# Kernel tuning notes

Measured on AMD Instinct MI355X. Metric: run time of the kernel, lower is better.

The kernel has to match this reference:

```python
import jax, jax.numpy as jnp
import numpy as np

Q_DIM = 1024
K_DIM = 1024
V_DIM = 1024
ATTEN_DIM = 1024
NUM_HEADS = 16
HEAD_DIM = ATTEN_DIM // NUM_HEADS
B, L = 4, 2048


def setup_inputs() -> dict:
    key = jax.random.key(0)
    ks = jax.random.split(key, 11)
    s = 0.02
    return {
        "query": jax.random.normal(ks[0], (B, L, Q_DIM), dtype=jnp.float32),
        "key":   jax.random.normal(ks[1], (B, L, K_DIM), dtype=jnp.float32),
        "value": jax.random.normal(ks[2], (B, L, V_DIM), dtype=jnp.float32),
        "Wq": jax.random.normal(ks[3], (Q_DIM, ATTEN_DIM), dtype=jnp.float32) * s,
        "bq": jnp.zeros((ATTEN_DIM,), dtype=jnp.float32),
        "Wk": jax.random.normal(ks[4], (K_DIM, ATTEN_DIM), dtype=jnp.float32) * s,
        "bk": jnp.zeros((ATTEN_DIM,), dtype=jnp.float32),
        "Wv": jax.random.normal(ks[5], (V_DIM, ATTEN_DIM), dtype=jnp.float32) * s,
        "bv": jnp.zeros((ATTEN_DIM,), dtype=jnp.float32),
        "Wo": jax.random.normal(ks[6], (ATTEN_DIM, V_DIM), dtype=jnp.float32) * s,
        "bo": jnp.zeros((V_DIM,), dtype=jnp.float32),
    }


def reference(query, key, value, Wq, bq, Wk, bk, Wv, bv, Wo, bo):
    # QKV projections
    q = query @ Wq + bq        # [B, L, A]
    k = key   @ Wk + bk        # [B, L, A]
    v = value @ Wv + bv        # [B, L, A]
    # split heads: [B, L, H, D]
    def split_heads(x):
        return x.reshape(x.shape[:-1] + (NUM_HEADS, HEAD_DIM))
    q, k, v = split_heads(q), split_heads(k), split_heads(v)
    scale = 1.0 / (HEAD_DIM ** 0.5)
    # scores: [B, H, Lq, Lk]
    scores = jnp.einsum("bqhd,bkhd->bhqk", q, k) * scale
    attn = jax.nn.softmax(scores, axis=-1)
    out = jnp.einsum("bhqk,bkhd->bqhd", attn, v)  # [B, Lq, H, D]
    out = out.reshape(out.shape[0], out.shape[1], ATTEN_DIM)
    return out @ Wo + bo
```

## Files before the change

kernel.cpp:

```cpp
#include <hip/hip_runtime.h>
#include <stdint.h>

#define L_SEQ 2048
#define BATCH 4
#define ADIM  1024
#define NH    16
#define HD    64

typedef __attribute__((ext_vector_type(8))) short bf16x8;
typedef __attribute__((ext_vector_type(4))) float f32x4;
typedef __attribute__((ext_vector_type(16))) float f32x16;
typedef __attribute__((ext_vector_type(2))) int i32x2;

__device__ __forceinline__ short f2bf(float f) {
    union { float f; unsigned u; } x; x.f = f;
    unsigned r = x.u + 0x7fffu + ((x.u >> 16) & 1u);
    return (short)(r >> 16);
}

__device__ __forceinline__ void async_ld16(void* lds, const void* g) {
    __builtin_amdgcn_global_load_lds(
        (const __attribute__((address_space(1))) void*)g,
        (__attribute__((address_space(3))) void*)lds, 16, 0, 0);
}

__device__ __forceinline__ int cvtpk_bf16(float a, float b) {
    int r;
    asm("v_cvt_pk_bf16_f32 %0, %1, %2" : "=v"(r) : "v"(a), "v"(b));
    return r;
}

__device__ __forceinline__ bf16x8 pack4(int a, int b, int c, int d) {
    union { int i[4]; bf16x8 v; } u;
    u.i[0] = a; u.i[1] = b; u.i[2] = c; u.i[3] = d;
    return u.v;
}

__global__ void cvt3_kernel(const float* __restrict__ s0, const float* __restrict__ s1,
                            const float* __restrict__ s2, short* __restrict__ dst, int n4) {
    int i = blockIdx.x * blockDim.x + threadIdx.x;
    if (i >= n4) return;
    int z = blockIdx.y;
    const float* src = (z == 0) ? s0 : (z == 1) ? s1 : s2;
    float4 v = reinterpret_cast<const float4*>(src)[i];
    short4 s;
    s.x = f2bf(v.x); s.y = f2bf(v.y); s.z = f2bf(v.z); s.w = f2bf(v.w);
    reinterpret_cast<short4*>(dst + (size_t)z * (BATCH * L_SEQ * ADIM))[i] = s;
}

__global__ void transpose4_kernel(const float* __restrict__ W0, const float* __restrict__ W1,
                                  const float* __restrict__ W2, const float* __restrict__ W3,
                                  short* __restrict__ outb) {
    __shared__ float t[32][33];
    int z = blockIdx.z;
    const float* in = (z == 0) ? W0 : (z == 1) ? W1 : (z == 2) ? W2 : W3;
    short* out = outb + (size_t)z * (ADIM * ADIM);
    int x  = blockIdx.x * 32 + threadIdx.x;
    int y0 = blockIdx.y * 32 + threadIdx.y;
#pragma unroll
    for (int j = 0; j < 4; ++j)
        t[threadIdx.y + 8 * j][threadIdx.x] = in[(y0 + 8 * j) * 1024 + x];
    __syncthreads();
    int x2 = blockIdx.y * 32 + threadIdx.x;
    int y2 = blockIdx.x * 32 + threadIdx.y;
#pragma unroll
    for (int j = 0; j < 4; ++j)
        out[(y2 + 8 * j) * 1024 + x2] = f2bf(t[threadIdx.x][threadIdx.y + 8 * j]);
}

__device__ __forceinline__ void gemm_core(const short* __restrict__ A,
                                          const short* __restrict__ BT,
                                          const float* __restrict__ bias,
                                          void* __restrict__ Cout,
                                          int mode, float scalemul,
                                          int m0, int n0) {
    const int K = 1024, N = 1024;
    __shared__ __align__(16) short smem[16384];
    int tid = threadIdx.x;
    int wave = tid >> 6, lane = tid & 63, quad = lane >> 4, l16 = lane & 15;
    int wm = wave & 1, wn = wave >> 1;
    f32x4 acc[4][4] = {};

    int row = tid >> 2, ck = tid & 3;
    const short* gA0 = A  + (size_t)(m0 + row) * K + ck * 8;
    const short* gA1 = gA0 + (size_t)64 * K;
    const short* gB0 = BT + (size_t)(n0 + row) * K + ck * 8;
    const short* gB1 = gB0 + (size_t)64 * K;
    int loA0 = tid * 8, loA1 = tid * 8 + 2048;
    int loB0 = tid * 8 + 4096, loB1 = tid * 8 + 6144;

    async_ld16(smem + loA0, gA0); async_ld16(smem + loA1, gA1);
    async_ld16(smem + loB0, gB0); async_ld16(smem + loB1, gB1);
    gA0 += 32; gA1 += 32; gB0 += 32; gB1 += 32;
    __syncthreads();

    int cur = 0;
    for (int t = 0; t < 32; ++t) {
        if (t < 31) {
            int off = (cur ^ 1) * 8192;
            async_ld16(smem + off + loA0, gA0); async_ld16(smem + off + loA1, gA1);
            async_ld16(smem + off + loB0, gB0); async_ld16(smem + off + loB1, gB1);
            gA0 += 32; gA1 += 32; gB0 += 32; gB1 += 32;
        }
        const short* Ab = smem + cur * 8192;
        const short* Bb = Ab + 4096;
        bf16x8 af[4], bfr[4];
#pragma unroll
        for (int mt = 0; mt < 4; ++mt)
            af[mt] = *(const bf16x8*)&Ab[(wm * 64 + mt * 16 + l16) * 32 + quad * 8];
#pragma unroll
        for (int nt = 0; nt < 4; ++nt)
            bfr[nt] = *(const bf16x8*)&Bb[(wn * 64 + nt * 16 + l16) * 32 + quad * 8];
#pragma unroll
        for (int mt = 0; mt < 4; ++mt)
#pragma unroll
            for (int nt = 0; nt < 4; ++nt)
                acc[mt][nt] = __builtin_amdgcn_mfma_f32_16x16x32_bf16(
                    af[mt], bfr[nt], acc[mt][nt], 0, 0, 0);
        __syncthreads();
        cur ^= 1;
    }

    if (mode == 0) {
#pragma unroll
        for (int nt = 0; nt < 4; ++nt) {
            int col = n0 + wn * 64 + nt * 16 + l16;
            float bv = bias[col];
#pragma unroll
            for (int mt = 0; mt < 4; ++mt)
#pragma unroll
                for (int r = 0; r < 4; ++r) {
                    int rw = m0 + wm * 64 + mt * 16 + quad * 4 + r;
                    ((short*)Cout)[(size_t)rw * N + col] = f2bf((acc[mt][nt][r] + bv) * scalemul);
                }
        }
    } else if (mode == 1) {
#pragma unroll
        for (int nt = 0; nt < 4; ++nt) {
            int col = n0 + wn * 64 + nt * 16 + l16;
            float bv = bias[col];
            int h = col >> 6, d = col & 63;
#pragma unroll
            for (int mt = 0; mt < 4; ++mt)
#pragma unroll
                for (int r = 0; r < 4; ++r) {
                    int rw = m0 + wm * 64 + mt * 16 + quad * 4 + r;
                    int b = rw >> 11, lk = rw & 2047;
                    ((short*)Cout)[(((size_t)b * NH + h) * HD + d) * L_SEQ + lk] =
                        f2bf(acc[mt][nt][r] + bv);
                }
        }
    } else {
#pragma unroll
        for (int nt = 0; nt < 4; ++nt) {
            int col = n0 + wn * 64 + nt * 16 + l16;
            float bv = bias[col];
#pragma unroll
            for (int mt = 0; mt < 4; ++mt)
#pragma unroll
                for (int r = 0; r < 4; ++r) {
                    int rw = m0 + wm * 64 + mt * 16 + quad * 4 + r;
                    ((float*)Cout)[(size_t)rw * N + col] = acc[mt][nt][r] + bv;
                }
        }
    }
}

__device__ __forceinline__ void gemm_swz(int& m0, int& n0) {
    int bid = blockIdx.y * 8 + blockIdx.x;
    int swz = (bid & 7) * 64 + (bid >> 3);
    n0 = (swz & 7) * 128;
    m0 = (swz >> 3) * 128;
}

__global__ __launch_bounds__(256, 4)
void gemm_one(const short* __restrict__ A, const short* __restrict__ BT,
              const float* __restrict__ bias, void* __restrict__ Cout,
              int mode, float scalemul) {
    int m0, n0; gemm_swz(m0, n0);
    gemm_core(A, BT, bias, Cout, mode, scalemul, m0, n0);
}

__global__ __launch_bounds__(256, 4)
void qkv_gemm(const short* __restrict__ Xbase, const short* __restrict__ WTbase,
              const float* __restrict__ bq, const float* __restrict__ bk,
              const float* __restrict__ bv,
              short* __restrict__ Qb, short* __restrict__ Kb, short* __restrict__ VTout,
              float qscale) {
    int z = blockIdx.z;
    const short* A  = Xbase + (size_t)z * (BATCH * L_SEQ * ADIM);
    const short* BT = WTbase + (size_t)z * (ADIM * ADIM);
    const float* bias = (z == 0) ? bq : (z == 1) ? bk : bv;
    void* out = (z == 0) ? (void*)Qb : (z == 1) ? (void*)Kb : (void*)VTout;
    int mode = (z == 2) ? 1 : 0;
    float sm = (z == 0) ? qscale : 1.0f;
    int m0, n0; gemm_swz(m0, n0);
    gemm_core(A, BT, bias, out, mode, sm, m0, n0);
}

__global__ __launch_bounds__(256, 4)
void attn_kernel(const short* __restrict__ Qb, const short* __restrict__ Kb,
                 const short* __restrict__ VT, short* __restrict__ Oout) {
    __shared__ __align__(16) short lds[16384];
    int tid = threadIdx.x;
    int wave = tid >> 6, lane = tid & 63;
    int r31 = lane & 31, hi = lane >> 5;

    int f = (blockIdx.z * NH + blockIdx.y) * (L_SEQ / 128) + blockIdx.x;
    int swz = (f & 7) * 128 + (f >> 3);
    int qb = swz & 15;
    int h  = (swz >> 4) & 15;
    int b  = swz >> 8;

    size_t qrow = (size_t)(b * L_SEQ + qb * 128 + wave * 32 + r31) * ADIM + h * HD;
    bf16x8 qf[4];
#pragma unroll
    for (int dc = 0; dc < 4; ++dc)
        qf[dc] = *(const bf16x8*)&Qb[qrow + dc * 16 + hi * 8];

    const short* Kbase = Kb + (size_t)b * L_SEQ * ADIM + h * HD;
    const short* Vbase = VT + ((size_t)(b * NH + h) * HD) * L_SEQ;
    const short* gp[4]; int step[4]; int ldso[4];
#pragma unroll
    for (int s = 0; s < 4; ++s) {
        int j = s * 256 + tid;
        ldso[s] = j * 8;
        if (j < 512) {
            int c = j >> 6, k = j & 63;
            gp[s] = Kbase + (size_t)k * ADIM + c * 8;
            step[s] = 64 * ADIM;
        } else {
            int jv = j - 512;
            int c = jv >> 6, d = jv & 63;
            gp[s] = Vbase + (size_t)d * L_SEQ + c * 8;
            step[s] = 64;
        }
    }

    f32x16 o0 = {}, o1 = {};
    f32x4 lp = {};

#pragma unroll
    for (int s = 0; s < 4; ++s) { async_ld16(lds + ldso[s], gp[s]); gp[s] += step[s]; }
    __syncthreads();

    int cur = 0;
    for (int t = 0; t < 32; ++t) {
        const short* kb_l = lds + cur * 8192;
        const short* vb_l = kb_l + 4096;
        if (t < 31) {
            short* dst = lds + (cur ^ 1) * 8192;
#pragma unroll
            for (int s = 0; s < 4; ++s) { async_ld16(dst + ldso[s], gp[s]); gp[s] += step[s]; }
        }
#pragma unroll
        for (int kt = 0; kt < 2; ++kt) {
            f32x16 sv = {};
            __builtin_amdgcn_s_setprio(1);
#pragma unroll
            for (int dc = 0; dc < 4; ++dc) {
                bf16x8 kf = *(const bf16x8*)&kb_l[(((dc << 1) + hi) * 64 + kt * 32 + r31) * 8];
                sv = __builtin_amdgcn_mfma_f32_32x32x16_bf16(kf, qf[dc], sv, 0, 0, 0);
            }
            __builtin_amdgcn_s_setprio(0);
#pragma unroll
            for (int r = 0; r < 16; ++r) sv[r] = __builtin_amdgcn_exp2f(sv[r]);
#pragma unroll
            for (int m = 0; m < 4; ++m)
#pragma unroll
                for (int j2 = 0; j2 < 4; ++j2) lp[j2] += sv[m * 4 + j2];

            int p0 = cvtpk_bf16(sv[0],  sv[1]);
            int p1 = cvtpk_bf16(sv[2],  sv[3]);
            int p2 = cvtpk_bf16(sv[4],  sv[5]);
            int p3 = cvtpk_bf16(sv[6],  sv[7]);
            int p4 = cvtpk_bf16(sv[8],  sv[9]);
            int p5 = cvtpk_bf16(sv[10], sv[11]);
            int p6 = cvtpk_bf16(sv[12], sv[13]);
            int p7 = cvtpk_bf16(sv[14], sv[15]);
            asm volatile("v_permlane32_swap_b32 %0, %1" : "+v"(p0), "+v"(p2));
            asm volatile("v_permlane32_swap_b32 %0, %1" : "+v"(p1), "+v"(p3));
            asm volatile("v_permlane32_swap_b32 %0, %1" : "+v"(p4), "+v"(p6));
            asm volatile("v_permlane32_swap_b32 %0, %1" : "+v"(p5), "+v"(p7));
            bf16x8 pf0 = pack4(p0, p1, p2, p3);
            bf16x8 pf1 = pack4(p4, p5, p6, p7);

            bf16x8 vf00 = *(const bf16x8*)&vb_l[((kt * 4 + hi)     * 64 + r31) * 8];
            bf16x8 vf01 = *(const bf16x8*)&vb_l[((kt * 4 + 2 + hi) * 64 + r31) * 8];
            bf16x8 vf10 = *(const bf16x8*)&vb_l[((kt * 4 + hi)     * 64 + 32 + r31) * 8];
            bf16x8 vf11 = *(const bf16x8*)&vb_l[((kt * 4 + 2 + hi) * 64 + 32 + r31) * 8];
            __builtin_amdgcn_s_setprio(1);
            o0 = __builtin_amdgcn_mfma_f32_32x32x16_bf16(vf00, pf0, o0, 0, 0, 0);
            o1 = __builtin_amdgcn_mfma_f32_32x32x16_bf16(vf10, pf0, o1, 0, 0, 0);
            o0 = __builtin_amdgcn_mfma_f32_32x32x16_bf16(vf01, pf1, o0, 0, 0, 0);
            o1 = __builtin_amdgcn_mfma_f32_32x32x16_bf16(vf11, pf1, o1, 0, 0, 0);
            __builtin_amdgcn_s_setprio(0);
        }
        __syncthreads();
        cur ^= 1;
    }

    float lsum = lp[0] + lp[1] + lp[2] + lp[3];
    lsum += __shfl_xor(lsum, 32);
    float inv = __builtin_amdgcn_rcpf(lsum);

    short* tile = lds + wave * (32 * 68);
#pragma unroll
    for (int dt = 0; dt < 2; ++dt)
#pragma unroll
        for (int g = 0; g < 4; ++g) {
            int d0 = dt * 32 + g * 8 + hi * 4;
            int pa, pb;
            if (dt == 0) {
                pa = cvtpk_bf16(o0[g * 4 + 0] * inv, o0[g * 4 + 1] * inv);
                pb = cvtpk_bf16(o0[g * 4 + 2] * inv, o0[g * 4 + 3] * inv);
            } else {
                pa = cvtpk_bf16(o1[g * 4 + 0] * inv, o1[g * 4 + 1] * inv);
                pb = cvtpk_bf16(o1[g * 4 + 2] * inv, o1[g * 4 + 3] * inv);
            }
            *(i32x2*)&tile[r31 * 68 + d0] = (i32x2){pa, pb};
        }
    __syncthreads();
    size_t obase = (size_t)(b * L_SEQ + qb * 128 + wave * 32) * ADIM + h * HD;
    int rr = lane >> 3, cc = lane & 7;
#pragma unroll
    for (int p = 0; p < 4; ++p) {
        int row = p * 8 + rr;
        bf16x8 v = *(const bf16x8*)&tile[row * 68 + cc * 8];
        *(bf16x8*)&Oout[obase + (size_t)row * ADIM + cc * 8] = v;
    }
}

extern "C" void kernel_launch(void* const* d_in, const int* in_sizes, int n_in,
                              void* d_out, int out_size, void* d_ws, size_t ws_size,
                              hipStream_t stream) {
    const float* query = (const float*)d_in[0];
    const float* keyp  = (const float*)d_in[1];
    const float* value = (const float*)d_in[2];
    const float* Wq = (const float*)d_in[3];
    const float* bq = (const float*)d_in[4];
    const float* Wk = (const float*)d_in[5];
    const float* bk = (const float*)d_in[6];
    const float* Wv = (const float*)d_in[7];
    const float* bv = (const float*)d_in[8];
    const float* Wo = (const float*)d_in[9];
    const float* bo = (const float*)d_in[10];

    const float QSCALE = 0.125f * 1.44269504f;
    const size_t MB = 1ull << 20;
    const int n4 = (BATCH * L_SEQ * ADIM) / 4;
    char* w = (char*)d_ws;
    dim3 tblk(32, 8);
    dim3 gemm_grid(ADIM / 128, (BATCH * L_SEQ) / 128);
    dim3 attn_grid(L_SEQ / 128, NH, BATCH);

    if (ws_size >= 104 * MB) {
        short* X0  = (short*)(w);
        short* WT  = (short*)(w + 48 * MB);
        short* VT  = (short*)(w + 56 * MB);
        short* Kb  = (short*)(w + 72 * MB);
        short* Qb  = (short*)(w + 88 * MB);
        short* AO  = X0;

        cvt3_kernel<<<dim3(n4 / 256, 3), 256, 0, stream>>>(query, keyp, value, X0, n4);
        transpose4_kernel<<<dim3(32, 32, 4), tblk, 0, stream>>>(Wq, Wk, Wv, Wo, WT);
        qkv_gemm<<<dim3(ADIM / 128, (BATCH * L_SEQ) / 128, 3), 256, 0, stream>>>(
            X0, WT, bq, bk, bv, Qb, Kb, VT, QSCALE);
        attn_kernel<<<attn_grid, 256, 0, stream>>>(Qb, Kb, VT, AO);
        gemm_one<<<gemm_grid, 256, 0, stream>>>(AO, WT + (size_t)3 * ADIM * ADIM, bo,
                                                d_out, 2, 1.0f);
    } else {
        short* X0  = (short*)(w);
        short* WT  = (short*)(w + 16 * MB);
        short* VT  = (short*)(w + 24 * MB);
        short* Kb  = (short*)(w + 40 * MB);
        short* Qb  = (short*)(w + 56 * MB);

        transpose4_kernel<<<dim3(32, 32, 4), tblk, 0, stream>>>(Wq, Wk, Wv, Wo, WT);
        cvt3_kernel<<<dim3(n4 / 256, 1), 256, 0, stream>>>(query, query, query, X0, n4);
        gemm_one<<<gemm_grid, 256, 0, stream>>>(X0, WT, bq, Qb, 0, QSCALE);
        cvt3_kernel<<<dim3(n4 / 256, 1), 256, 0, stream>>>(keyp, keyp, keyp, X0, n4);
        gemm_one<<<gemm_grid, 256, 0, stream>>>(X0, WT + (size_t)ADIM * ADIM, bk, Kb, 0, 1.0f);
        cvt3_kernel<<<dim3(n4 / 256, 1), 256, 0, stream>>>(value, value, value, X0, n4);
        gemm_one<<<gemm_grid, 256, 0, stream>>>(X0, WT + (size_t)2 * ADIM * ADIM, bv, VT, 1, 1.0f);
        attn_kernel<<<attn_grid, 256, 0, stream>>>(Qb, Kb, VT, X0);
        gemm_one<<<gemm_grid, 256, 0, stream>>>(X0, WT + (size_t)3 * ADIM * ADIM, bo,
                                                d_out, 2, 1.0f);
    }
}
```

Baseline: 333.7 us.

## Rework GEMM to 256x128 tiles with 8 waves and triple-buffered K=64 pipeline

Replaces the 128x128, 4-wave GEMM core with a 256x128 tile computed by 512 threads (8 waves). Each stage loads K=64 with a k-major LDS layout and a three-deep async load ring, overlapped through explicit vmcnt waits and barriers. MFMA bursts get raised wave priority via s_setprio. The aim is more operand reuse per global byte and better latency hiding in the QKV and output projections. The cost is 144KB of LDS per block, which limits occupancy, and fewer blocks in the grid.

```diff
diff --git a/kernel.cpp b/kernel.cpp
--- a/kernel.cpp
+++ b/kernel.cpp
@@ -68,83 +68,120 @@
         out[(y2 + 8 * j) * 1024 + x2] = f2bf(t[threadIdx.x][threadIdx.y + 8 * j]);
 }
 
-__device__ __forceinline__ void gemm_core(const short* __restrict__ A,
-                                          const short* __restrict__ BT,
-                                          const float* __restrict__ bias,
-                                          void* __restrict__ Cout,
-                                          int mode, float scalemul,
-                                          int m0, int n0) {
+__device__ __forceinline__ void gemm8_core(const short* __restrict__ A,
+                                           const short* __restrict__ BT,
+                                           const float* __restrict__ bias,
+                                           void* __restrict__ Cout,
+                                           int mode, float scalemul,
+                                           int m0, int n0) {
     const int K = 1024, N = 1024;
-    __shared__ __align__(16) short smem[16384];
+    __shared__ __align__(16) short smem[3 * 24576];
     int tid = threadIdx.x;
     int wave = tid >> 6, lane = tid & 63, quad = lane >> 4, l16 = lane & 15;
-    int wm = wave & 1, wn = wave >> 1;
-    f32x4 acc[4][4] = {};
-
-    int row = tid >> 2, ck = tid & 3;
-    const short* gA0 = A  + (size_t)(m0 + row) * K + ck * 8;
-    const short* gA1 = gA0 + (size_t)64 * K;
-    const short* gB0 = BT + (size_t)(n0 + row) * K + ck * 8;
-    const short* gB1 = gB0 + (size_t)64 * K;
-    int loA0 = tid * 8, loA1 = tid * 8 + 2048;
-    int loB0 = tid * 8 + 4096, loB1 = tid * 8 + 6144;
-
-    async_ld16(smem + loA0, gA0); async_ld16(smem + loA1, gA1);
-    async_ld16(smem + loB0, gB0); async_ld16(smem + loB1, gB1);
-    gA0 += 32; gA1 += 32; gB0 += 32; gB1 += 32;
-    __syncthreads();
+    int wm = wave >> 2, wn = wave & 3;
+    int bh = wn >> 1;
+
+    f32x4 acc[8][2] = {};
+
+    const short* gp[6]; int ldo[6];
+#pragma unroll
+    for (int s = 0; s < 4; ++s) {
+        int c = wn * 64 + s * 256 + lane;
+        int row = c & 127, kq = c >> 7;
+        gp[s]  = A + (size_t)(m0 + wm * 128 + row) * K + kq * 8;
+        ldo[s] = wm * 8192 + c * 8;
+    }
+#pragma unroll
+    for (int s = 0; s < 2; ++s) {
+        int c = (wm * 2 + (wn & 1)) * 64 + s * 256 + lane;
+        int row = c & 63, kq = c >> 6;
+        gp[4 + s]  = BT + (size_t)(n0 + bh * 64 + row) * K + kq * 8;
+        ldo[4 + s] = 16384 + bh * 4096 + c * 8;
+    }
+
+#pragma unroll
+    for (int s = 0; s < 6; ++s) { async_ld16(smem + ldo[s], gp[s]); gp[s] += 64; }
+#pragma unroll
+    for (int s = 0; s < 6; ++s) { async_ld16(smem + 24576 + ldo[s], gp[s]); gp[s] += 64; }
+    asm volatile("s_waitcnt vmcnt(6)" ::: "memory");
+    __builtin_amdgcn_sched_barrier(0);
+    __builtin_amdgcn_s_barrier();
 
     int cur = 0;
-    for (int t = 0; t < 32; ++t) {
-        if (t < 31) {
-            int off = (cur ^ 1) * 8192;
-            async_ld16(smem + off + loA0, gA0); async_ld16(smem + off + loA1, gA1);
-            async_ld16(smem + off + loB0, gB0); async_ld16(smem + off + loB1, gB1);
-            gA0 += 32; gA1 += 32; gB0 += 32; gB1 += 32;
-        }
-        const short* Ab = smem + cur * 8192;
-        const short* Bb = Ab + 4096;
-        bf16x8 af[4], bfr[4];
-#pragma unroll
-        for (int mt = 0; mt < 4; ++mt)
-            af[mt] = *(const bf16x8*)&Ab[(wm * 64 + mt * 16 + l16) * 32 + quad * 8];
-#pragma unroll
-        for (int nt = 0; nt < 4; ++nt)
-            bfr[nt] = *(const bf16x8*)&Bb[(wn * 64 + nt * 16 + l16) * 32 + quad * 8];
-#pragma unroll
-        for (int mt = 0; mt < 4; ++mt)
-#pragma unroll
-            for (int nt = 0; nt < 4; ++nt)
-                acc[mt][nt] = __builtin_amdgcn_mfma_f32_16x16x32_bf16(
-                    af[mt], bfr[nt], acc[mt][nt], 0, 0, 0);
-        __syncthreads();
-        cur ^= 1;
+    for (int t = 0; t < 16; ++t) {
+        int nxt2 = cur + 2; if (nxt2 >= 3) nxt2 -= 3;
+        if (t + 2 < 16) {
+#pragma unroll
+            for (int s = 0; s < 6; ++s) {
+                async_ld16(smem + nxt2 * 24576 + ldo[s], gp[s]);
+                gp[s] += 64;
+            }
+        }
+        const short* Ab = smem + cur * 24576 + wm * 8192;
+        const short* Bb = smem + cur * 24576 + 16384 + bh * 4096;
+        bf16x8 bfr[2][2];
+#pragma unroll
+        for (int nt = 0; nt < 2; ++nt)
+#pragma unroll
+            for (int kk = 0; kk < 2; ++kk)
+                bfr[nt][kk] = *(const bf16x8*)
+                    &Bb[(kk * 4 + quad) * 512 + ((wn & 1) * 32 + nt * 16 + l16) * 8];
+#pragma unroll
+        for (int ph = 0; ph < 2; ++ph) {
+            bf16x8 af[4][2];
+#pragma unroll
+            for (int mt = 0; mt < 4; ++mt)
+#pragma unroll
+                for (int kk = 0; kk < 2; ++kk)
+                    af[mt][kk] = *(const bf16x8*)
+                        &Ab[(kk * 4 + quad) * 1024 + (ph * 64 + mt * 16 + l16) * 8];
+            __builtin_amdgcn_s_setprio(1);
+#pragma unroll
+            for (int mt = 0; mt < 4; ++mt)
+#pragma unroll
+                for (int nt = 0; nt < 2; ++nt) {
+                    acc[ph * 4 + mt][nt] = __builtin_amdgcn_mfma_f32_16x16x32_bf16(
+                        af[mt][0], bfr[nt][0], acc[ph * 4 + mt][nt], 0, 0, 0);
+                    acc[ph * 4 + mt][nt] = __builtin_amdgcn_mfma_f32_16x16x32_bf16(
+                        af[mt][1], bfr[nt][1], acc[ph * 4 + mt][nt], 0, 0, 0);
+                }
+            __builtin_amdgcn_s_setprio(0);
+            if (ph == 0) __builtin_amdgcn_s_barrier();
+        }
+        if (t < 14) {
+            asm volatile("s_waitcnt vmcnt(6)" ::: "memory");
+        } else if (t == 14) {
+            asm volatile("s_waitcnt vmcnt(0)" ::: "memory");
+        }
+        __builtin_amdgcn_sched_barrier(0);
+        __builtin_amdgcn_s_barrier();
+        cur = (cur + 1 == 3) ? 0 : cur + 1;
     }
 
     if (mode == 0) {
 #pragma unroll
-        for (int nt = 0; nt < 4; ++nt) {
-            int col = n0 + wn * 64 + nt * 16 + l16;
+        for (int nt = 0; nt < 2; ++nt) {
+            int col = n0 + wn * 32 + nt * 16 + l16;
             float bv = bias[col];
 #pragma unroll
-            for (int mt = 0; mt < 4; ++mt)
+            for (int mt = 0; mt < 8; ++mt)
 #pragma unroll
                 for (int r = 0; r < 4; ++r) {
-                    int rw = m0 + wm * 64 + mt * 16 + quad * 4 + r;
+                    int rw = m0 + wm * 128 + mt * 16 + quad * 4 + r;
                     ((short*)Cout)[(size_t)rw * N + col] = f2bf((acc[mt][nt][r] + bv) * scalemul);
                 }
         }
     } else if (mode == 1) {
 #pragma unroll
-        for (int nt = 0; nt < 4; ++nt) {
-            int col = n0 + wn * 64 + nt * 16 + l16;
+        for (int nt = 0; nt < 2; ++nt) {
+            int col = n0 + wn * 32 + nt * 16 + l16;
             float bv = bias[col];
             int h = col >> 6, d = col & 63;
 #pragma unroll
-            for (int mt = 0; mt < 4; ++mt)
+            for (int mt = 0; mt < 8; ++mt)
 #pragma unroll
                 for (int r = 0; r < 4; ++r) {
-                    int rw = m0 + wm * 64 + mt * 16 + quad * 4 + r;
+                    int rw = m0 + wm * 128 + mt * 16 + quad * 4 + r;
                     int b = rw >> 11, lk = rw & 2047;
                     ((short*)Cout)[(((size_t)b * NH + h) * HD + d) * L_SEQ + lk] =
                         f2bf(acc[mt][nt][r] + bv);
@@ -152,36 +189,36 @@
         }
     } else {
 #pragma unroll
-        for (int nt = 0; nt < 4; ++nt) {
-            int col = n0 + wn * 64 + nt * 16 + l16;
+        for (int nt = 0; nt < 2; ++nt) {
+            int col = n0 + wn * 32 + nt * 16 + l16;
             float bv = bias[col];
 #pragma unroll
-            for (int mt = 0; mt < 4; ++mt)
+            for (int mt = 0; mt < 8; ++mt)
 #pragma unroll
                 for (int r = 0; r < 4; ++r) {
-                    int rw = m0 + wm * 64 + mt * 16 + quad * 4 + r;
+                    int rw = m0 + wm * 128 + mt * 16 + quad * 4 + r;
                     ((float*)Cout)[(size_t)rw * N + col] = acc[mt][nt][r] + bv;
                 }
         }
     }
 }
 
-__device__ __forceinline__ void gemm_swz(int& m0, int& n0) {
+__device__ __forceinline__ void gemm8_swz(int& m0, int& n0) {
     int bid = blockIdx.y * 8 + blockIdx.x;
-    int swz = (bid & 7) * 64 + (bid >> 3);
+    int swz = (bid & 7) * 32 + (bid >> 3);
     n0 = (swz & 7) * 128;
-    m0 = (swz >> 3) * 128;
-}
-
-__global__ __launch_bounds__(256, 4)
+    m0 = (swz >> 3) * 256;
+}
+
+__global__ __launch_bounds__(512, 2)
 void gemm_one(const short* __restrict__ A, const short* __restrict__ BT,
               const float* __restrict__ bias, void* __restrict__ Cout,
               int mode, float scalemul) {
-    int m0, n0; gemm_swz(m0, n0);
-    gemm_core(A, BT, bias, Cout, mode, scalemul, m0, n0);
-}
-
-__global__ __launch_bounds__(256, 4)
+    int m0, n0; gemm8_swz(m0, n0);
+    gemm8_core(A, BT, bias, Cout, mode, scalemul, m0, n0);
+}
+
+__global__ __launch_bounds__(512, 2)
 void qkv_gemm(const short* __restrict__ Xbase, const short* __restrict__ WTbase,
               const float* __restrict__ bq, const float* __restrict__ bk,
               const float* __restrict__ bv,
@@ -194,8 +231,8 @@
     void* out = (z == 0) ? (void*)Qb : (z == 1) ? (void*)Kb : (void*)VTout;
     int mode = (z == 2) ? 1 : 0;
     float sm = (z == 0) ? qscale : 1.0f;
-    int m0, n0; gemm_swz(m0, n0);
-    gemm_core(A, BT, bias, out, mode, sm, m0, n0);
+    int m0, n0; gemm8_swz(m0, n0);
+    gemm8_core(A, BT, bias, out, mode, sm, m0, n0);
 }
 
 __global__ __launch_bounds__(256, 4)
@@ -351,7 +388,7 @@
     const int n4 = (BATCH * L_SEQ * ADIM) / 4;
     char* w = (char*)d_ws;
     dim3 tblk(32, 8);
-    dim3 gemm_grid(ADIM / 128, (BATCH * L_SEQ) / 128);
+    dim3 gemm_grid(ADIM / 128, (BATCH * L_SEQ) / 256);
     dim3 attn_grid(L_SEQ / 128, NH, BATCH);
 
     if (ws_size >= 104 * MB) {
@@ -364,10 +401,10 @@
 
         cvt3_kernel<<<dim3(n4 / 256, 3), 256, 0, stream>>>(query, keyp, value, X0, n4);
         transpose4_kernel<<<dim3(32, 32, 4), tblk, 0, stream>>>(Wq, Wk, Wv, Wo, WT);
-        qkv_gemm<<<dim3(ADIM / 128, (BATCH * L_SEQ) / 128, 3), 256, 0, stream>>>(
+        qkv_gemm<<<dim3(ADIM / 128, (BATCH * L_SEQ) / 256, 3), 512, 0, stream>>>(
             X0, WT, bq, bk, bv, Qb, Kb, VT, QSCALE);
         attn_kernel<<<attn_grid, 256, 0, stream>>>(Qb, Kb, VT, AO);
-        gemm_one<<<gemm_grid, 256, 0, stream>>>(AO, WT + (size_t)3 * ADIM * ADIM, bo,
+        gemm_one<<<gemm_grid, 512, 0, stream>>>(AO, WT + (size_t)3 * ADIM * ADIM, bo,
                                                 d_out, 2, 1.0f);
     } else {
         short* X0  = (short*)(w);
@@ -378,13 +415,13 @@
 
         transpose4_kernel<<<dim3(32, 32, 4), tblk, 0, stream>>>(Wq, Wk, Wv, Wo, WT);
         cvt3_kernel<<<dim3(n4 / 256, 1), 256, 0, stream>>>(query, query, query, X0, n4);
-        gemm_one<<<gemm_grid, 256, 0, stream>>>(X0, WT, bq, Qb, 0, QSCALE);
+        gemm_one<<<gemm_grid, 512, 0, stream>>>(X0, WT, bq, Qb, 0, QSCALE);
         cvt3_kernel<<<dim3(n4 / 256, 1), 256, 0, stream>>>(keyp, keyp, keyp, X0, n4);
-        gemm_one<<<gemm_grid, 256, 0, stream>>>(X0, WT + (size_t)ADIM * ADIM, bk, Kb, 0, 1.0f);
+        gemm_one<<<gemm_grid, 512, 0, stream>>>(X0, WT + (size_t)ADIM * ADIM, bk, Kb, 0, 1.0f);
         cvt3_kernel<<<dim3(n4 / 256, 1), 256, 0, stream>>>(value, value, value, X0, n4);
-        gemm_one<<<gemm_grid, 256, 0, stream>>>(X0, WT + (size_t)2 * ADIM * ADIM, bv, VT, 1, 1.0f);
+        gemm_one<<<gemm_grid, 512, 0, stream>>>(X0, WT + (size_t)2 * ADIM * ADIM, bv, VT, 1, 1.0f);
         attn_kernel<<<attn_grid, 256, 0, stream>>>(Qb, Kb, VT, X0);
-        gemm_one<<<gemm_grid, 256, 0, stream>>>(X0, WT + (size_t)3 * ADIM * ADIM, bo,
+        gemm_one<<<gemm_grid, 512, 0, stream>>>(X0, WT + (size_t)3 * ADIM * ADIM, bo,
                                                 d_out, 2, 1.0f);
     }
 }
```

Measured after the change: 370.5 us. +11.0%, slower.

## Stage K-transpose epilogue through LDS and compute softmax row sums via MFMA

Applied to the files above, without the earlier changes.

The transposed (mode 1) GEMM epilogue now packs bf16 results into a per-wave LDS tile and writes 16-byte contiguous chunks along the sequence dimension, replacing scattered 2-byte strided global stores. In the attention kernel, the VALU accumulation of exp values for the softmax denominator is replaced by extra MFMAs against an all-ones matrix. This accumulates the denominator from the bf16-rounded probabilities, which matches what multiplies V. It adds two MFMAs per tile, one more 16-register accumulator, and extra LDS traffic in the epilogue.

```diff
diff --git a/kernel.cpp b/kernel.cpp
--- a/kernel.cpp
+++ b/kernel.cpp
@@ -135,20 +135,29 @@
                 }
         }
     } else if (mode == 1) {
+        short* tw = smem + wave * 1120;
+        int rbase = m0 + wm * 64;
+        int bidx = rbase >> 11, lk0 = rbase & 2047;
 #pragma unroll
         for (int nt = 0; nt < 4; ++nt) {
-            int col = n0 + wn * 64 + nt * 16 + l16;
-            float bv = bias[col];
-            int h = col >> 6, d = col & 63;
-#pragma unroll
-            for (int mt = 0; mt < 4; ++mt)
-#pragma unroll
-                for (int r = 0; r < 4; ++r) {
-                    int rw = m0 + wm * 64 + mt * 16 + quad * 4 + r;
-                    int b = rw >> 11, lk = rw & 2047;
-                    ((short*)Cout)[(((size_t)b * NH + h) * HD + d) * L_SEQ + lk] =
-                        f2bf(acc[mt][nt][r] + bv);
-                }
+            int col0 = n0 + wn * 64 + nt * 16;
+            int h = col0 >> 6, d0 = col0 & 63;
+            float bv = bias[col0 + l16];
+#pragma unroll
+            for (int mt = 0; mt < 4; ++mt) {
+                int a0 = cvtpk_bf16(acc[mt][nt][0] + bv, acc[mt][nt][1] + bv);
+                int a1 = cvtpk_bf16(acc[mt][nt][2] + bv, acc[mt][nt][3] + bv);
+                *(int*)&tw[l16 * 70 + mt * 16 + quad * 4]     = a0;
+                *(int*)&tw[l16 * 70 + mt * 16 + quad * 4 + 2] = a1;
+            }
+            int dl = lane >> 2;
+            short* dst = (short*)Cout +
+                (((size_t)bidx * NH + h) * HD + d0 + dl) * L_SEQ + lk0;
+#pragma unroll
+            for (int p = 0; p < 2; ++p) {
+                int ch = (lane & 3) + p * 4;
+                *(bf16x8*)&dst[ch * 8] = *(const bf16x8*)&tw[dl * 70 + ch * 8];
+            }
         }
     } else {
 #pragma unroll
@@ -237,8 +246,8 @@
         }
     }
 
-    f32x16 o0 = {}, o1 = {};
-    f32x4 lp = {};
+    f32x16 o0 = {}, o1 = {}, lacc = {};
+    const bf16x8 ones = pack4(0x3F803F80, 0x3F803F80, 0x3F803F80, 0x3F803F80);
 
 #pragma unroll
     for (int s = 0; s < 4; ++s) { async_ld16(lds + ldso[s], gp[s]); gp[s] += step[s]; }
@@ -265,10 +274,6 @@
             __builtin_amdgcn_s_setprio(0);
 #pragma unroll
             for (int r = 0; r < 16; ++r) sv[r] = __builtin_amdgcn_exp2f(sv[r]);
-#pragma unroll
-            for (int m = 0; m < 4; ++m)
-#pragma unroll
-                for (int j2 = 0; j2 < 4; ++j2) lp[j2] += sv[m * 4 + j2];
 
             int p0 = cvtpk_bf16(sv[0],  sv[1]);
             int p1 = cvtpk_bf16(sv[2],  sv[3]);
@@ -292,17 +297,17 @@
             __builtin_amdgcn_s_setprio(1);
             o0 = __builtin_amdgcn_mfma_f32_32x32x16_bf16(vf00, pf0, o0, 0, 0, 0);
             o1 = __builtin_amdgcn_mfma_f32_32x32x16_bf16(vf10, pf0, o1, 0, 0, 0);
+            lacc = __builtin_amdgcn_mfma_f32_32x32x16_bf16(ones, pf0, lacc, 0, 0, 0);
             o0 = __builtin_amdgcn_mfma_f32_32x32x16_bf16(vf01, pf1, o0, 0, 0, 0);
             o1 = __builtin_amdgcn_mfma_f32_32x32x16_bf16(vf11, pf1, o1, 0, 0, 0);
+            lacc = __builtin_amdgcn_mfma_f32_32x32x16_bf16(ones, pf1, lacc, 0, 0, 0);
             __builtin_amdgcn_s_setprio(0);
         }
         __syncthreads();
         cur ^= 1;
     }
 
-    float lsum = lp[0] + lp[1] + lp[2] + lp[3];
-    lsum += __shfl_xor(lsum, 32);
-    float inv = __builtin_amdgcn_rcpf(lsum);
+    float inv = __builtin_amdgcn_rcpf(lacc[0]);
 
     short* tile = lds + wave * (32 * 68);
 #pragma unroll
```

New measurement: 335.2 us, median of 2. Within noise of the previous version (+0.4%).
